# Kernel optimization log

Measured on AMD Instinct MI355X. Metric: run time of the kernel, lower is better.

The kernel has to match this reference:

```python
import jax, jax.numpy as jnp
import numpy as np

DIM = 768
NUM_HEADS = 12
HEAD_DIM = DIM // NUM_HEADS
SCALE = HEAD_DIM ** -0.5


def setup_inputs() -> dict:
    key = jax.random.key(0)
    k1, k2, k3, k4 = jax.random.split(key, 4)
    B, H, W = 8, 32, 32
    x = jax.random.normal(k1, (B, H, W, DIM), dtype=jnp.float32)
    s = DIM ** -0.5
    w_qkv = jax.random.normal(k2, (DIM, 3 * DIM), dtype=jnp.float32) * s
    w_proj = jax.random.normal(k3, (DIM, DIM), dtype=jnp.float32) * s
    b_proj = jax.random.normal(k4, (DIM,), dtype=jnp.float32) * 0.01
    return {"x": x, "w_qkv": w_qkv, "w_proj": w_proj, "b_proj": b_proj}


def reference(x, w_qkv, w_proj, b_proj):
    B, H, W, C = x.shape
    N = H * W
    qkv = (x.reshape(B, N, C) @ w_qkv).reshape(B, N, 3, NUM_HEADS, HEAD_DIM)
    q, k, v = jnp.moveaxis(qkv, 2, 0)  # each (B, N, h, d)
    # scores: (B, h, N, N)
    attn = jnp.einsum('bnhd,bmhd->bhnm', q * SCALE, k)
    attn = jax.nn.softmax(attn, axis=-1)
    out = jnp.einsum('bhnm,bmhd->bnhd', attn, v).reshape(B, H, W, C)
    return out @ w_proj + b_proj
```

## Files before the change

kernel.cpp:

```cpp
#include <hip/hip_runtime.h>

typedef _Float16 half_t;
typedef __attribute__((ext_vector_type(4))) _Float16 half4;
typedef __attribute__((ext_vector_type(8))) _Float16 half8;
typedef __attribute__((ext_vector_type(4))) float floatx4;

#define MFMA_F16(A,B,C)  __builtin_amdgcn_mfma_f32_16x16x32_f16(A,B,C,0,0,0)

typedef __attribute__((address_space(1))) const void gvoid_t;
typedef __attribute__((address_space(3))) void svoid_t;

__device__ __forceinline__ void async_copy16(const half_t* g, half_t* l) {
    __builtin_amdgcn_global_load_lds((gvoid_t*)g, (svoid_t*)l, 16, 0, 0);
}

__global__ __launch_bounds__(256)
void prep_kernel(const float* __restrict__ x, const float* __restrict__ w_qkv,
                 const float* __restrict__ w_proj, half_t* __restrict__ xh,
                 half_t* __restrict__ wqkvT, half_t* __restrict__ wprojT)
{
    __shared__ half_t tile[64 * 65];
    const int id = blockIdx.x, tid = threadIdx.x;
    if (id < 6144) {
        size_t e = (size_t)id * 1024 + tid * 4;
        float4 f = *(const float4*)(x + e);
        half4 h = { (half_t)f.x, (half_t)f.y, (half_t)f.z, (half_t)f.w };
        *(half4*)(xh + e) = h;
        return;
    }
    const float* src; half_t* dst; int lds, tr0, tc0;
    if (id < 6576) { int t = id - 6144; src = w_qkv; dst = wqkvT; lds = 2304;
                     tr0 = (t / 36) * 64; tc0 = (t % 36) * 64; }
    else           { int t = id - 6576; src = w_proj; dst = wprojT; lds = 768;
                     tr0 = (t / 12) * 64; tc0 = (t % 12) * 64; }
    #pragma unroll
    for (int i = 0; i < 4; i++) {
        int e = tid + i * 256, r = e >> 4, c4 = (e & 15) << 2;
        float4 f = *(const float4*)(src + (size_t)(tr0 + r) * lds + tc0 + c4);
        tile[(c4 + 0) * 65 + r] = (half_t)f.x;
        tile[(c4 + 1) * 65 + r] = (half_t)f.y;
        tile[(c4 + 2) * 65 + r] = (half_t)f.z;
        tile[(c4 + 3) * 65 + r] = (half_t)f.w;
    }
    __syncthreads();
    #pragma unroll
    for (int i = 0; i < 4; i++) {
        int e = tid + i * 256, c = e >> 4, r4 = (e & 15) << 2;
        half4 h = { tile[c * 65 + r4], tile[c * 65 + r4 + 1],
                    tile[c * 65 + r4 + 2], tile[c * 65 + r4 + 3] };
        *(half4*)(dst + (size_t)(tc0 + c) * 768 + tr0 + r4) = h;
    }
}

__global__ __launch_bounds__(256, 2)
void gemm_qkv(const half_t* __restrict__ A, const half_t* __restrict__ Bt,
              half_t* __restrict__ q_ws, half_t* __restrict__ k_ws,
              half_t* __restrict__ v_ws)
{
    __shared__ half_t As[128 * 64];
    __shared__ half_t Bs[256 * 64];

    const int lin  = blockIdx.x;
    const int xcd  = lin & 7, rest = lin >> 3;
    const int m0 = ((rest / 9) * 8 + xcd) * 128;
    const int n0 = (rest % 9) * 256;

    const int tid  = threadIdx.x;
    const int lane = tid & 63;
    const int w    = tid >> 6;
    const int quad = lane >> 4, l16 = lane & 15;
    const int lrow = lane >> 3;
    const int lcc  = (lane & 7) ^ lrow;
    const int xsw  = l16 & 7;

    const half_t* Ag = A  + (size_t)(m0 + w * 32 + lrow) * 768 + lcc * 8;
    const half_t* Bg = Bt + (size_t)(n0 + w * 64 + lrow) * 768 + lcc * 8;

    floatx4 acc[8][4];
    #pragma unroll
    for (int i = 0; i < 8; i++)
        #pragma unroll
        for (int j = 0; j < 4; j++) acc[i][j] = (floatx4)0.0f;

    for (int k0 = 0; k0 < 768; k0 += 64) {
        #pragma unroll
        for (int i = 0; i < 4; i++)
            async_copy16(Ag + (size_t)(i * 8) * 768 + k0, As + (w * 4 + i) * 512);
        #pragma unroll
        for (int i = 0; i < 8; i++)
            async_copy16(Bg + (size_t)(i * 8) * 768 + k0, Bs + (w * 8 + i) * 512);
        __syncthreads();

        #pragma unroll
        for (int ks = 0; ks < 2; ks++) {
            const int co = (((ks << 2) + quad) ^ xsw) * 8;
            half8 a[8], b[4];
            #pragma unroll
            for (int mi = 0; mi < 8; mi++)
                a[mi] = *(const half8*)(As + (mi * 16 + l16) * 64 + co);
            #pragma unroll
            for (int ni = 0; ni < 4; ni++)
                b[ni] = *(const half8*)(Bs + (w * 64 + ni * 16 + l16) * 64 + co);
            #pragma unroll
            for (int mi = 0; mi < 8; mi++)
                #pragma unroll
                for (int ni = 0; ni < 4; ni++)
                    acc[mi][ni] = MFMA_F16(a[mi], b[ni], acc[mi][ni]);
        }
        __syncthreads();
    }

    const int sel  = n0 / 768;
    const int rem0 = n0 - sel * 768;
    const int hh   = (rem0 >> 6) + w;
    const int bb   = m0 >> 10;
    const int t0   = m0 & 1023;
    const size_t base = (size_t)(bb * 12 + hh) * 65536;

    if (sel == 0) {
        #pragma unroll
        for (int mi = 0; mi < 8; mi++)
            #pragma unroll
            for (int ni = 0; ni < 4; ni++) {
                int d   = ni * 16 + l16;
                int tok = t0 + mi * 16 + quad * 4;
                half4 hv = { (half_t)(acc[mi][ni][0] * 0.125f),
                             (half_t)(acc[mi][ni][1] * 0.125f),
                             (half_t)(acc[mi][ni][2] * 0.125f),
                             (half_t)(acc[mi][ni][3] * 0.125f) };
                *(half4*)(q_ws + base + (size_t)d * 1024 + tok) = hv;
            }
    } else if (sel == 1) {
        #pragma unroll
        for (int mi = 0; mi < 8; mi++)
            #pragma unroll
            for (int ni = 0; ni < 4; ni++) {
                int d = ni * 16 + l16;
                #pragma unroll
                for (int r = 0; r < 4; r++) {
                    int tok = t0 + mi * 16 + quad * 4 + r;
                    k_ws[base + (size_t)tok * 64 + d] = (half_t)acc[mi][ni][r];
                }
            }
    } else {
        #pragma unroll
        for (int mi = 0; mi < 8; mi++)
            #pragma unroll
            for (int ni = 0; ni < 4; ni++) {
                int d    = ni * 16 + l16;
                int tokb = (t0 + mi * 16 + quad * 4) & ~31;
                int tokp = tokb | (quad << 3) | ((mi & 1) << 2);
                half4 hv = { (half_t)acc[mi][ni][0], (half_t)acc[mi][ni][1],
                             (half_t)acc[mi][ni][2], (half_t)acc[mi][ni][3] };
                *(half4*)(v_ws + base + (size_t)d * 1024 + tokp) = hv;
            }
    }
}

__global__ __launch_bounds__(256, 2)
void gemm_proj(const half_t* __restrict__ A, const half_t* __restrict__ Bt,
               float* __restrict__ Cout, const float* __restrict__ bias)
{
    __shared__ half_t As[128 * 64];
    __shared__ half_t Bs[128 * 64];

    const int lin  = blockIdx.x;
    const int xcd  = lin & 7, rest = lin >> 3;
    const int m0 = ((rest / 6) * 8 + xcd) * 128;
    const int n0 = (rest % 6) * 128;

    const int tid  = threadIdx.x;
    const int lane = tid & 63;
    const int w    = tid >> 6;
    const int wm   = w >> 1, wn = w & 1;
    const int quad = lane >> 4, l16 = lane & 15;
    const int lrow = lane >> 3;
    const int lcc  = (lane & 7) ^ lrow;
    const int xsw  = l16 & 7;

    const half_t* Ag = A  + (size_t)(m0 + w * 32 + lrow) * 768 + lcc * 8;
    const half_t* Bg = Bt + (size_t)(n0 + w * 32 + lrow) * 768 + lcc * 8;

    floatx4 acc[4][4];
    #pragma unroll
    for (int i = 0; i < 4; i++)
        #pragma unroll
        for (int j = 0; j < 4; j++) acc[i][j] = (floatx4)0.0f;

    for (int k0 = 0; k0 < 768; k0 += 64) {
        #pragma unroll
        for (int i = 0; i < 4; i++) {
            async_copy16(Ag + (size_t)(i * 8) * 768 + k0, As + (w * 4 + i) * 512);
            async_copy16(Bg + (size_t)(i * 8) * 768 + k0, Bs + (w * 4 + i) * 512);
        }
        __syncthreads();

        #pragma unroll
        for (int ks = 0; ks < 2; ks++) {
            const int co = (((ks << 2) + quad) ^ xsw) * 8;
            half8 a[4], b[4];
            #pragma unroll
            for (int mi = 0; mi < 4; mi++)
                a[mi] = *(const half8*)(As + (wm * 64 + mi * 16 + l16) * 64 + co);
            #pragma unroll
            for (int ni = 0; ni < 4; ni++)
                b[ni] = *(const half8*)(Bs + (wn * 64 + ni * 16 + l16) * 64 + co);
            #pragma unroll
            for (int mi = 0; mi < 4; mi++)
                #pragma unroll
                for (int ni = 0; ni < 4; ni++)
                    acc[mi][ni] = MFMA_F16(a[mi], b[ni], acc[mi][ni]);
        }
        __syncthreads();
    }

    float bias_v[4];
    #pragma unroll
    for (int ni = 0; ni < 4; ni++)
        bias_v[ni] = bias[n0 + wn * 64 + ni * 16 + l16];
    float* scratch = (w < 2 ? (float*)As : (float*)Bs) + (w & 1) * 1152;
    #pragma unroll
    for (int mi = 0; mi < 4; mi++) {
        #pragma unroll
        for (int ni = 0; ni < 4; ni++)
            #pragma unroll
            for (int r = 0; r < 4; r++)
                scratch[(quad * 4 + r) * 72 + ni * 16 + l16] =
                    acc[mi][ni][r] + bias_v[ni];
        #pragma unroll
        for (int i = 0; i < 4; i++) {
            int f = quad + i * 4;
            float4 v4 = *(const float4*)(scratch + l16 * 72 + f * 4);
            int gm = m0 + wm * 64 + mi * 16 + l16;
            *(float4*)(Cout + (size_t)gm * 768 + n0 + wn * 64 + f * 4) = v4;
        }
    }
}

__global__ __launch_bounds__(256, 3)
void attn_kernel(const half_t* __restrict__ qT, const half_t* __restrict__ k,
                 const half_t* __restrict__ vT, half_t* __restrict__ a_ws)
{
    __shared__ __align__(16) half_t Kb[2][4096];
    __shared__ __align__(16) half_t Vb[2][4096];
    __shared__ __align__(16) half_t Qs[64 * 128];

    const int lin  = blockIdx.x;
    const int xcd  = lin & 7, rest = lin >> 3;
    const int qc   = rest & 7;
    const int bh   = (rest >> 3) * 8 + xcd;

    const int tid  = threadIdx.x;
    const int lane = tid & 63;
    const int w    = tid >> 6;
    const int quad = lane >> 4, l16 = lane & 15;

    const half_t* qg = qT + (size_t)bh * 65536;
    const half_t* kg = k  + (size_t)bh * 65536;
    const half_t* vg = vT + (size_t)bh * 65536;

    const int srow = lane >> 3;
    const int sch  = (lane & 7) ^ srow;

    #pragma unroll
    for (int j = 0; j < 4; j++) {
        int d0 = w * 16 + j * 4;
        async_copy16(qg + (size_t)(d0 + (lane >> 4)) * 1024 + qc * 128 + (lane & 15) * 8,
                     &Qs[d0 * 128]);
    }
    #pragma unroll
    for (int j = 0; j < 2; j++) {
        int row = j * 32 + w * 8;
        async_copy16(kg + (size_t)(row + srow) * 64 + sch * 8, &Kb[0][row * 64]);
        async_copy16(vg + (size_t)(row + srow) * 1024 + sch * 8, &Vb[0][row * 64]);
    }
    __syncthreads();

    half8 qf[2][2];
    #pragma unroll
    for (int T = 0; T < 2; T++)
        #pragma unroll
        for (int ks = 0; ks < 2; ks++)
            #pragma unroll
            for (int j = 0; j < 8; j++)
                qf[T][ks][j] = Qs[(ks * 32 + quad * 8 + j) * 128
                                  + T * 64 + w * 16 + l16];

    floatx4 acc_o[2][4];
    floatx4 lacc[2];
    #pragma unroll
    for (int T = 0; T < 2; T++) {
        lacc[T] = (floatx4)0.0f;
        #pragma unroll
        for (int dt = 0; dt < 4; dt++) acc_o[T][dt] = (floatx4)0.0f;
    }

    const int xsw = l16 & 7;
    const half8 vone = { (half_t)1.0f, (half_t)1.0f, (half_t)1.0f, (half_t)1.0f,
                         (half_t)1.0f, (half_t)1.0f, (half_t)1.0f, (half_t)1.0f };

    for (int kt = 0; kt < 16; kt++) {
        const int cb = kt & 1;
        __syncthreads();
        if (kt < 15) {
            #pragma unroll
            for (int j = 0; j < 2; j++) {
                int row = j * 32 + w * 8;
                async_copy16(kg + (size_t)((kt + 1) * 64 + row + srow) * 64 + sch * 8,
                             &Kb[cb ^ 1][row * 64]);
                async_copy16(vg + (size_t)(row + srow) * 1024 + (kt + 1) * 64 + sch * 8,
                             &Vb[cb ^ 1][row * 64]);
            }
        }
        const half_t* Kc = Kb[cb];
        const half_t* Vc = Vb[cb];

        floatx4 sc[2][4];
        #pragma unroll
        for (int T = 0; T < 2; T++)
            #pragma unroll
            for (int mt = 0; mt < 4; mt++) sc[T][mt] = (floatx4)0.0f;
        #pragma unroll
        for (int ks = 0; ks < 2; ks++)
            #pragma unroll
            for (int mt = 0; mt < 4; mt++) {
                half8 kf = *(const half8*)(Kc + (mt * 16 + l16) * 64
                                              + (((ks << 2) + quad) ^ xsw) * 8);
                sc[0][mt] = MFMA_F16(kf, qf[0][ks], sc[0][mt]);
                sc[1][mt] = MFMA_F16(kf, qf[1][ks], sc[1][mt]);
            }

        half8 pa[2][2];
        #pragma unroll
        for (int T = 0; T < 2; T++)
            #pragma unroll
            for (int g = 0; g < 2; g++) {
                half8 ph;
                #pragma unroll
                for (int r = 0; r < 4; r++) ph[r]     = (half_t)__expf(sc[T][2 * g][r]);
                #pragma unroll
                for (int r = 0; r < 4; r++) ph[4 + r] = (half_t)__expf(sc[T][2 * g + 1][r]);
                pa[T][g] = ph;
            }

        #pragma unroll
        for (int g = 0; g < 2; g++) {
            lacc[0] = MFMA_F16(pa[0][g], vone, lacc[0]);
            lacc[1] = MFMA_F16(pa[1][g], vone, lacc[1]);
            #pragma unroll
            for (int dt = 0; dt < 4; dt++) {
                half8 vb = *(const half8*)(Vc + (dt * 16 + l16) * 64
                                              + ((((g << 2) + quad) ^ xsw) << 3));
                acc_o[0][dt] = MFMA_F16(pa[0][g], vb, acc_o[0][dt]);
                acc_o[1][dt] = MFMA_F16(pa[1][g], vb, acc_o[1][dt]);
            }
        }
    }

    const int b = bh / 12, h = bh - (bh / 12) * 12;
    #pragma unroll
    for (int T = 0; T < 2; T++)
        #pragma unroll
        for (int r = 0; r < 4; r++) {
            float inv = 1.0f / lacc[T][r];
            int n = qc * 128 + T * 64 + w * 16 + quad * 4 + r;
            half_t* op = a_ws + ((size_t)(b * 1024 + n)) * 768 + h * 64;
            #pragma unroll
            for (int dt = 0; dt < 4; dt++)
                op[dt * 16 + l16] = (half_t)(acc_o[T][dt][r] * inv);
        }
}

extern "C" void kernel_launch(void* const* d_in, const int* in_sizes, int n_in,
                              void* d_out, int out_size, void* d_ws, size_t ws_size,
                              hipStream_t stream)
{
    (void)in_sizes; (void)n_in; (void)out_size; (void)ws_size;
    const float* x      = (const float*)d_in[0];
    const float* w_qkv  = (const float*)d_in[1];
    const float* w_proj = (const float*)d_in[2];
    const float* b_proj = (const float*)d_in[3];
    float* out = (float*)d_out;

    half_t* ws     = (half_t*)d_ws;
    half_t* q_ws   = ws;
    half_t* k_ws   = ws + 6291456;
    half_t* v_ws   = ws + 2 * 6291456;
    half_t* xh     = ws + 3 * 6291456;
    half_t* wqkvT  = ws + 4 * 6291456;
    half_t* wprojT = wqkvT + 1769472;
    half_t* a_ws   = xh;

    prep_kernel<<<dim3(6720), dim3(256), 0, stream>>>(x, w_qkv, w_proj, xh, wqkvT, wprojT);
    gemm_qkv<<<dim3(576), dim3(256), 0, stream>>>(xh, wqkvT, q_ws, k_ws, v_ws);
    attn_kernel<<<dim3(768), dim3(256), 0, stream>>>(q_ws, k_ws, v_ws, a_ws);
    gemm_proj<<<dim3(384), dim3(256), 0, stream>>>(a_ws, wprojT, out, b_proj);
}
```

Before: 185.5 us.

## Double-buffer QKV GEMM with 128x192 tiles and 2x2 warp layout

Restructures the QKV projection GEMM to use a 128x192 output tile with K-step 32 and double-buffered LDS, so the next slice's async global-to-LDS copies are issued while the current slice runs MFMAs. Warps are arranged 2x2 instead of 1x4, and a new XOR swizzle lays out LDS rows for conflict-free reads. The grid grows from 576 to 768 blocks with a target of 3 blocks per CU, aiming for more occupancy and better latency hiding. The risks are more barriers per K (24 steps instead of 12) and output tiles that now straddle head boundaries, which complicates the epilogue addressing.

```diff
diff --git a/kernel.cpp b/kernel.cpp
--- a/kernel.cpp
+++ b/kernel.cpp
@@ -52,78 +52,93 @@
     }
 }
 
-__global__ __launch_bounds__(256, 2)
+__global__ __launch_bounds__(256, 3)
 void gemm_qkv(const half_t* __restrict__ A, const half_t* __restrict__ Bt,
               half_t* __restrict__ q_ws, half_t* __restrict__ k_ws,
               half_t* __restrict__ v_ws)
 {
-    __shared__ half_t As[128 * 64];
-    __shared__ half_t Bs[256 * 64];
+    __shared__ half_t As[2][128 * 32];
+    __shared__ half_t Bs[2][192 * 32];
 
     const int lin  = blockIdx.x;
     const int xcd  = lin & 7, rest = lin >> 3;
-    const int m0 = ((rest / 9) * 8 + xcd) * 128;
-    const int n0 = (rest % 9) * 256;
+    const int m0 = ((rest / 12) * 8 + xcd) * 128;
+    const int n0 = (rest % 12) * 192;
 
     const int tid  = threadIdx.x;
     const int lane = tid & 63;
     const int w    = tid >> 6;
+    const int wm   = w >> 1, wn = w & 1;
     const int quad = lane >> 4, l16 = lane & 15;
-    const int lrow = lane >> 3;
-    const int lcc  = (lane & 7) ^ lrow;
-    const int xsw  = l16 & 7;
-
-    const half_t* Ag = A  + (size_t)(m0 + w * 32 + lrow) * 768 + lcc * 8;
-    const half_t* Bg = Bt + (size_t)(n0 + w * 64 + lrow) * 768 + lcc * 8;
-
-    floatx4 acc[8][4];
-    #pragma unroll
-    for (int i = 0; i < 8; i++)
-        #pragma unroll
-        for (int j = 0; j < 4; j++) acc[i][j] = (floatx4)0.0f;
-
-    for (int k0 = 0; k0 < 768; k0 += 64) {
-        #pragma unroll
-        for (int i = 0; i < 4; i++)
-            async_copy16(Ag + (size_t)(i * 8) * 768 + k0, As + (w * 4 + i) * 512);
-        #pragma unroll
-        for (int i = 0; i < 8; i++)
-            async_copy16(Bg + (size_t)(i * 8) * 768 + k0, Bs + (w * 8 + i) * 512);
+
+    const int b0p = (lane ^ (lane >> 2) ^ (lane >> 4)) & 1;
+    const int b1p = ((lane >> 1) ^ (lane >> 3)) & 1;
+    const int b2p = ((lane >> 2) ^ (lane >> 4)) & 1;
+    const int row_log = ((lane >> 2) & 0xC) | ((lane >> 2) & 2) | b2p;
+    const int q_log   = (b1p << 1) | b0p;
+
+    const int foff = ((((l16 << 2) | quad) ^ (l16 & 7)) << 3);
+
+    const half_t* a_src0 = A  + (size_t)(m0 + (w*2+0)*16 + row_log) * 768 + q_log*8;
+    const half_t* a_src1 = A  + (size_t)(m0 + (w*2+1)*16 + row_log) * 768 + q_log*8;
+    const half_t* b_src0 = Bt + (size_t)(n0 + (w*3+0)*16 + row_log) * 768 + q_log*8;
+    const half_t* b_src1 = Bt + (size_t)(n0 + (w*3+1)*16 + row_log) * 768 + q_log*8;
+    const half_t* b_src2 = Bt + (size_t)(n0 + (w*3+2)*16 + row_log) * 768 + q_log*8;
+
+    floatx4 acc[4][6];
+    #pragma unroll
+    for (int i = 0; i < 4; i++)
+        #pragma unroll
+        for (int j = 0; j < 6; j++) acc[i][j] = (floatx4)0.0f;
+
+    async_copy16(a_src0, &As[0][(w*2+0)*512]);
+    async_copy16(a_src1, &As[0][(w*2+1)*512]);
+    async_copy16(b_src0, &Bs[0][(w*3+0)*512]);
+    async_copy16(b_src1, &Bs[0][(w*3+1)*512]);
+    async_copy16(b_src2, &Bs[0][(w*3+2)*512]);
+    __syncthreads();
+
+    for (int t = 0; t < 24; ++t) {
+        const int cur = t & 1;
+        if (t < 23) {
+            const int ko = (t + 1) * 32;
+            async_copy16(a_src0 + ko, &As[cur ^ 1][(w*2+0)*512]);
+            async_copy16(a_src1 + ko, &As[cur ^ 1][(w*2+1)*512]);
+            async_copy16(b_src0 + ko, &Bs[cur ^ 1][(w*3+0)*512]);
+            async_copy16(b_src1 + ko, &Bs[cur ^ 1][(w*3+1)*512]);
+            async_copy16(b_src2 + ko, &Bs[cur ^ 1][(w*3+2)*512]);
+        }
+        half8 a[4], b[6];
+        #pragma unroll
+        for (int mi = 0; mi < 4; mi++)
+            a[mi] = *(const half8*)(&As[cur][(wm*4 + mi) * 512 + foff]);
+        #pragma unroll
+        for (int ni = 0; ni < 6; ni++)
+            b[ni] = *(const half8*)(&Bs[cur][(wn*6 + ni) * 512 + foff]);
+        #pragma unroll
+        for (int mi = 0; mi < 4; mi++)
+            #pragma unroll
+            for (int ni = 0; ni < 6; ni++)
+                acc[mi][ni] = MFMA_F16(a[mi], b[ni], acc[mi][ni]);
         __syncthreads();
-
-        #pragma unroll
-        for (int ks = 0; ks < 2; ks++) {
-            const int co = (((ks << 2) + quad) ^ xsw) * 8;
-            half8 a[8], b[4];
-            #pragma unroll
-            for (int mi = 0; mi < 8; mi++)
-                a[mi] = *(const half8*)(As + (mi * 16 + l16) * 64 + co);
-            #pragma unroll
-            for (int ni = 0; ni < 4; ni++)
-                b[ni] = *(const half8*)(Bs + (w * 64 + ni * 16 + l16) * 64 + co);
-            #pragma unroll
-            for (int mi = 0; mi < 8; mi++)
-                #pragma unroll
-                for (int ni = 0; ni < 4; ni++)
-                    acc[mi][ni] = MFMA_F16(a[mi], b[ni], acc[mi][ni]);
-        }
-        __syncthreads();
-    }
-
-    const int sel  = n0 / 768;
+    }
+
+    const int sel  = (n0 >= 1536) ? 2 : (n0 >= 768 ? 1 : 0);
     const int rem0 = n0 - sel * 768;
-    const int hh   = (rem0 >> 6) + w;
     const int bb   = m0 >> 10;
     const int t0   = m0 & 1023;
-    const size_t base = (size_t)(bb * 12 + hh) * 65536;
+    const int rw   = wm * 64;
 
     if (sel == 0) {
         #pragma unroll
-        for (int mi = 0; mi < 8; mi++)
-            #pragma unroll
-            for (int ni = 0; ni < 4; ni++) {
-                int d   = ni * 16 + l16;
-                int tok = t0 + mi * 16 + quad * 4;
+        for (int mi = 0; mi < 4; mi++)
+            #pragma unroll
+            for (int ni = 0; ni < 6; ni++) {
+                int cb = rem0 + wn*96 + ni*16;
+                int hh = cb >> 6;
+                int d  = (cb & 63) + l16;
+                size_t base = (size_t)(bb * 12 + hh) * 65536;
+                int tok = t0 + rw + mi*16 + quad*4;
                 half4 hv = { (half_t)(acc[mi][ni][0] * 0.125f),
                              (half_t)(acc[mi][ni][1] * 0.125f),
                              (half_t)(acc[mi][ni][2] * 0.125f),
@@ -132,23 +147,29 @@
             }
     } else if (sel == 1) {
         #pragma unroll
-        for (int mi = 0; mi < 8; mi++)
-            #pragma unroll
-            for (int ni = 0; ni < 4; ni++) {
-                int d = ni * 16 + l16;
+        for (int mi = 0; mi < 4; mi++)
+            #pragma unroll
+            for (int ni = 0; ni < 6; ni++) {
+                int cb = rem0 + wn*96 + ni*16;
+                int hh = cb >> 6;
+                int d  = (cb & 63) + l16;
+                size_t base = (size_t)(bb * 12 + hh) * 65536;
                 #pragma unroll
                 for (int r = 0; r < 4; r++) {
-                    int tok = t0 + mi * 16 + quad * 4 + r;
+                    int tok = t0 + rw + mi*16 + quad*4 + r;
                     k_ws[base + (size_t)tok * 64 + d] = (half_t)acc[mi][ni][r];
                 }
             }
     } else {
         #pragma unroll
-        for (int mi = 0; mi < 8; mi++)
-            #pragma unroll
-            for (int ni = 0; ni < 4; ni++) {
-                int d    = ni * 16 + l16;
-                int tokb = (t0 + mi * 16 + quad * 4) & ~31;
+        for (int mi = 0; mi < 4; mi++)
+            #pragma unroll
+            for (int ni = 0; ni < 6; ni++) {
+                int cb = rem0 + wn*96 + ni*16;
+                int hh = cb >> 6;
+                int d  = (cb & 63) + l16;
+                size_t base = (size_t)(bb * 12 + hh) * 65536;
+                int tokb = t0 + rw + (mi >> 1) * 32;
                 int tokp = tokb | (quad << 3) | ((mi & 1) << 2);
                 half4 hv = { (half_t)acc[mi][ni][0], (half_t)acc[mi][ni][1],
                              (half_t)acc[mi][ni][2], (half_t)acc[mi][ni][3] };
@@ -392,7 +413,7 @@
     half_t* a_ws   = xh;
 
     prep_kernel<<<dim3(6720), dim3(256), 0, stream>>>(x, w_qkv, w_proj, xh, wqkvT, wprojT);
-    gemm_qkv<<<dim3(576), dim3(256), 0, stream>>>(xh, wqkvT, q_ws, k_ws, v_ws);
+    gemm_qkv<<<dim3(768), dim3(256), 0, stream>>>(xh, wqkvT, q_ws, k_ws, v_ws);
     attn_kernel<<<dim3(768), dim3(256), 0, stream>>>(q_ws, k_ws, v_ws, a_ws);
     gemm_proj<<<dim3(384), dim3(256), 0, stream>>>(a_ws, wprojT, out, b_proj);
 }
```

New measurement: 178.4 us. -3.8%, faster.
